# Kernel tuning notes

Measured on AMD Instinct MI355X. Metric: run time of the kernel, lower is better.

The kernel has to match this reference:

```python
import jax, jax.numpy as jnp
import numpy as np

EPSILON = 1e-36


def setup_inputs() -> dict:
    key = jax.random.key(0)
    k1, k2, k3, k4 = jax.random.split(key, 4)
    n, in_dim, out_dim = 8192, 128, 128
    x = jax.random.normal(k1, (n, in_dim), dtype=jnp.float32)
    # xavier-uniform-like scale for W_real
    limit = float(np.sqrt(6.0 / (in_dim + out_dim)))
    W_real = jax.random.uniform(k2, (in_dim, out_dim), dtype=jnp.float32, minval=-limit, maxval=limit)
    W_imag = jax.random.uniform(k3, (in_dim, out_dim), dtype=jnp.float32, minval=-0.1, maxval=0.1)
    G = jax.random.uniform(k4, (in_dim, out_dim), dtype=jnp.float32, minval=0.0, maxval=1.0)
    return {"x": x, "W_real": W_real, "W_imag": W_imag, "G": G}


def reference(x, W_real, W_imag, G):
    Gc = jnp.clip(G, 0.0, 1.0)                                   # (i,o)
    # R: (n,i,o) = |x| gated toward 1 by (1-G)
    R = (jnp.abs(x) + EPSILON)[:, :, None] * Gc[None] + (1.0 - Gc)[None]
    # K: pi where x<0, gated by G
    K = jnp.pi * (x < 0).astype(x.dtype)[:, :, None] * Gc[None]  # (n,i,o)
    logR = jnp.log(R)
    A = jnp.einsum('nio,io->no', logR, W_real) - jnp.einsum('nio,io->no', K, W_imag)
    B = jnp.einsum('nio,io->no', logR, W_imag) + jnp.einsum('nio,io->no', K, W_real)
    return jnp.exp(A) * jnp.cos(B)
```

## Files before the change

kernel.cpp:

```cpp
#include <hip/hip_runtime.h>
#include <math.h>


#define NROWS 8192
#define DIM   128
#define NB    8
#define PI_F  3.14159265358979323846f

typedef float v2f __attribute__((ext_vector_type(2)));

static __device__ __forceinline__ v2f vfma2(v2f a, v2f b, v2f c) {
#if defined(__has_builtin) && __has_builtin(__builtin_elementwise_fma)
    return __builtin_elementwise_fma(a, b, c);
#else
    v2f r; r.x = fmaf(a.x, b.x, c.x); r.y = fmaf(a.y, b.y, c.y); return r;
#endif
}

__global__ __launch_bounds__(256) void prep_kernel(
    const float* __restrict__ x, const float* __restrict__ Wr,
    const float* __restrict__ Wi, const float* __restrict__ G,
    float2* __restrict__ amps, float4* __restrict__ w4)
{
    int idx = blockIdx.x * 256 + threadIdx.x;
    int stride = gridDim.x * 256;
    for (int t = idx; t < NROWS * DIM; t += stride) {
        float xv = x[t];
        float am1 = fabsf(xv) - 1.0f;
        float ps  = (xv < 0.0f) ? PI_F : 0.0f;
        amps[t] = make_float2(am1, ps);
    }
    for (int t = idx; t < DIM * DIM; t += stride) {
        float g = fminf(fmaxf(G[t], 0.0f), 1.0f);
        w4[t] = make_float4(g, Wr[t], Wi[t], 0.0f);
    }
}

__global__ __launch_bounds__(128) void main_kernel(
    const float2* __restrict__ amps, const float4* __restrict__ w4,
    float* __restrict__ out)
{
    const int o = threadIdx.x;
    const int nbase = blockIdx.x * NB;

    v2f accL[NB], accK[NB];
#pragma unroll
    for (int r = 0; r < NB; ++r) { accL[r] = (v2f){0.f, 0.f}; accK[r] = (v2f){0.f, 0.f}; }

    const float2* ap = amps + (size_t)nbase * DIM;

#pragma unroll 2
    for (int i = 0; i < DIM; ++i) {
        float4 w = w4[i * DIM + o];
        const float g = w.x, wr = w.y, wi = w.z;
        const v2f wv = {wr, wi};
        const v2f gv = {g * wi, g * wr};
#pragma unroll
        for (int r = 0; r < NB; ++r) {
            float2 a = ap[r * DIM + i];
            float t  = fmaf(a.x, g, 1.0f);
            float l  = __log2f(t);
            v2f lv = {l, l};
            v2f pv = {a.y, a.y};
            accL[r] = vfma2(lv, wv, accL[r]);
            accK[r] = vfma2(pv, gv, accK[r]);
        }
    }

    const float LN2 = 0.69314718055994530942f;
#pragma unroll
    for (int r = 0; r < NB; ++r) {
        float A = fmaf(LN2, accL[r].x, -accK[r].x);
        float B = fmaf(LN2, accL[r].y,  accK[r].y);
        out[(size_t)(nbase + r) * DIM + o] = expf(A) * cosf(B);
    }
}

__global__ __launch_bounds__(128) void fallback_kernel(
    const float* __restrict__ x, const float* __restrict__ Wr,
    const float* __restrict__ Wi, const float* __restrict__ G,
    float* __restrict__ out)
{
    const int o = threadIdx.x;
    const int nbase = blockIdx.x * NB;

    v2f accL[NB], accK[NB];
#pragma unroll
    for (int r = 0; r < NB; ++r) { accL[r] = (v2f){0.f, 0.f}; accK[r] = (v2f){0.f, 0.f}; }

    for (int i = 0; i < DIM; ++i) {
        float g  = fminf(fmaxf(G[i * DIM + o], 0.0f), 1.0f);
        float wr = Wr[i * DIM + o];
        float wi = Wi[i * DIM + o];
        const v2f wv = {wr, wi};
        const v2f gv = {g * wi, g * wr};
#pragma unroll
        for (int r = 0; r < NB; ++r) {
            float xv  = x[(size_t)(nbase + r) * DIM + i];
            float am1 = fabsf(xv) - 1.0f;
            float ps  = (xv < 0.0f) ? PI_F : 0.0f;
            float t   = fmaf(am1, g, 1.0f);
            float l   = __log2f(t);
            v2f lv = {l, l};
            v2f pv = {ps, ps};
            accL[r] = vfma2(lv, wv, accL[r]);
            accK[r] = vfma2(pv, gv, accK[r]);
        }
    }

    const float LN2 = 0.69314718055994530942f;
#pragma unroll
    for (int r = 0; r < NB; ++r) {
        float A = fmaf(LN2, accL[r].x, -accK[r].x);
        float B = fmaf(LN2, accL[r].y,  accK[r].y);
        out[(size_t)(nbase + r) * DIM + o] = expf(A) * cosf(B);
    }
}

extern "C" void kernel_launch(void* const* d_in, const int* in_sizes, int n_in,
                              void* d_out, int out_size, void* d_ws, size_t ws_size,
                              hipStream_t stream) {
    const float* x  = (const float*)d_in[0];
    const float* Wr = (const float*)d_in[1];
    const float* Wi = (const float*)d_in[2];
    const float* G  = (const float*)d_in[3];
    float* out = (float*)d_out;

    const size_t amps_bytes = (size_t)NROWS * DIM * sizeof(float2);
    const size_t w4_bytes   = (size_t)DIM * DIM * sizeof(float4);
    if (ws_size >= amps_bytes + w4_bytes) {
        float2* amps = (float2*)d_ws;
        float4* w4   = (float4*)((char*)d_ws + amps_bytes);
        prep_kernel<<<1024, 256, 0, stream>>>(x, Wr, Wi, G, amps, w4);
        main_kernel<<<NROWS / NB, 128, 0, stream>>>(amps, w4, out);
    } else {
        fallback_kernel<<<NROWS / NB, 128, 0, stream>>>(x, Wr, Wi, G, out);
    }
}
```

Before: 104.2 us.

## Fuse x preprocessing into main kernel via shared memory, split rows across 512 threads

The per-element x transform (|x|-1 and the sign phase) moves out of a separate global-memory pass and into the main kernel, which stages 8 rows in LDS per block. This drops the write and re-read of an 8 MB intermediate buffer. Each block now has 512 threads, and each thread computes 2 rows for one output column instead of 8. That raises thread-level parallelism but loads each weight float4 four times per block, once per row group.

Measured after the change: 98.12 us. 5.8% less time.

```diff
diff --git a/kernel.cpp b/kernel.cpp
--- a/kernel.cpp
+++ b/kernel.cpp
@@ -4,7 +4,9 @@
 
 #define NROWS 8192
 #define DIM   128
-#define NB    8
+#define RPB   8
+#define NT    512
+#define RPT   2
 #define PI_F  3.14159265358979323846f
 
 typedef float v2f __attribute__((ext_vector_type(2)));
@@ -17,103 +19,76 @@
 #endif
 }
 
-__global__ __launch_bounds__(256) void prep_kernel(
-    const float* __restrict__ x, const float* __restrict__ Wr,
-    const float* __restrict__ Wi, const float* __restrict__ G,
-    float2* __restrict__ amps, float4* __restrict__ w4)
+__global__ __launch_bounds__(256) void prep_w(
+    const float* __restrict__ Wr, const float* __restrict__ Wi,
+    const float* __restrict__ G, float4* __restrict__ w4)
 {
-    int idx = blockIdx.x * 256 + threadIdx.x;
-    int stride = gridDim.x * 256;
-    for (int t = idx; t < NROWS * DIM; t += stride) {
-        float xv = x[t];
-        float am1 = fabsf(xv) - 1.0f;
-        float ps  = (xv < 0.0f) ? PI_F : 0.0f;
-        amps[t] = make_float2(am1, ps);
-    }
-    for (int t = idx; t < DIM * DIM; t += stride) {
+    int t = blockIdx.x * 256 + threadIdx.x;
+    if (t < DIM * DIM) {
         float g = fminf(fmaxf(G[t], 0.0f), 1.0f);
         w4[t] = make_float4(g, Wr[t], Wi[t], 0.0f);
     }
 }
 
-__global__ __launch_bounds__(128) void main_kernel(
-    const float2* __restrict__ amps, const float4* __restrict__ w4,
-    float* __restrict__ out)
+template <bool PACKED>
+__global__ __launch_bounds__(NT, 8) void main_kernel(
+    const float* __restrict__ x, const float4* __restrict__ w4,
+    const float* __restrict__ Wr, const float* __restrict__ Wi,
+    const float* __restrict__ G, float* __restrict__ out)
 {
-    const int o = threadIdx.x;
-    const int nbase = blockIdx.x * NB;
+    __shared__ float2 amps[RPB * DIM];
+    const int tid   = threadIdx.x;
+    const int o     = tid & (DIM - 1);
+    const int q     = tid >> 7;
+    const int nbase = blockIdx.x * RPB;
 
-    v2f accL[NB], accK[NB];
-#pragma unroll
-    for (int r = 0; r < NB; ++r) { accL[r] = (v2f){0.f, 0.f}; accK[r] = (v2f){0.f, 0.f}; }
+    {
+        const float2* xr = (const float2*)(x + (size_t)nbase * DIM);
+        float2 v = xr[tid];
+        float4 s;
+        s.x = fabsf(v.x) - 1.0f;  s.y = (v.x < 0.0f) ? PI_F : 0.0f;
+        s.z = fabsf(v.y) - 1.0f;  s.w = (v.y < 0.0f) ? PI_F : 0.0f;
+        ((float4*)amps)[tid] = s;
+    }
+    __syncthreads();
 
-    const float2* ap = amps + (size_t)nbase * DIM;
+    const float2* ap = amps + q * (RPT * DIM);
+    v2f aL0 = {0.f,0.f}, aK0 = {0.f,0.f}, aL1 = {0.f,0.f}, aK1 = {0.f,0.f};
 
-#pragma unroll 2
+#pragma unroll 4
     for (int i = 0; i < DIM; ++i) {
-        float4 w = w4[i * DIM + o];
-        const float g = w.x, wr = w.y, wi = w.z;
+        float g, wr, wi;
+        if (PACKED) {
+            float4 w = w4[i * DIM + o];
+            g = w.x; wr = w.y; wi = w.z;
+        } else {
+            g  = fminf(fmaxf(G[i * DIM + o], 0.0f), 1.0f);
+            wr = Wr[i * DIM + o]; wi = Wi[i * DIM + o];
+        }
         const v2f wv = {wr, wi};
         const v2f gv = {g * wi, g * wr};
-#pragma unroll
-        for (int r = 0; r < NB; ++r) {
-            float2 a = ap[r * DIM + i];
-            float t  = fmaf(a.x, g, 1.0f);
-            float l  = __log2f(t);
-            v2f lv = {l, l};
-            v2f pv = {a.y, a.y};
-            accL[r] = vfma2(lv, wv, accL[r]);
-            accK[r] = vfma2(pv, gv, accK[r]);
-        }
+        float2 a0 = ap[i];
+        float2 a1 = ap[DIM + i];
+        float t0 = fmaf(a0.x, g, 1.0f);
+        float t1 = fmaf(a1.x, g, 1.0f);
+        float l0 = __log2f(t0);
+        float l1 = __log2f(t1);
+        aL0 = vfma2((v2f){l0, l0},     wv, aL0);
+        aK0 = vfma2((v2f){a0.y, a0.y}, gv, aK0);
+        aL1 = vfma2((v2f){l1, l1},     wv, aL1);
+        aK1 = vfma2((v2f){a1.y, a1.y}, gv, aK1);
     }
 
     const float LN2 = 0.69314718055994530942f;
-#pragma unroll
-    for (int r = 0; r < NB; ++r) {
-        float A = fmaf(LN2, accL[r].x, -accK[r].x);
-        float B = fmaf(LN2, accL[r].y,  accK[r].y);
-        out[(size_t)(nbase + r) * DIM + o] = expf(A) * cosf(B);
+    {
+        float A = fmaf(LN2, aL0.x, -aK0.x);
+        float B = fmaf(LN2, aL0.y,  aK0.y);
+        out[(size_t)(nbase + q * RPT) * DIM + o] = expf(A) * cosf(B);
     }
-}
-
-__global__ __launch_bounds__(128) void fallback_kernel(
-    const float* __restrict__ x, const float* __restrict__ Wr,
-    const float* __restrict__ Wi, const float* __restrict__ G,
-    float* __restrict__ out)
-{
-    const int o = threadIdx.x;
-    const int nbase = blockIdx.x * NB;
-
-    v2f accL[NB], accK[NB];
-#pragma unroll
-    for (int r = 0; r < NB; ++r) { accL[r] = (v2f){0.f, 0.f}; accK[r] = (v2f){0.f, 0.f}; }
-
-    for (int i = 0; i < DIM; ++i) {
-        float g  = fminf(fmaxf(G[i * DIM + o], 0.0f), 1.0f);
-        float wr = Wr[i * DIM + o];
-        float wi = Wi[i * DIM + o];
-        const v2f wv = {wr, wi};
-        const v2f gv = {g * wi, g * wr};
-#pragma unroll
-        for (int r = 0; r < NB; ++r) {
-            float xv  = x[(size_t)(nbase + r) * DIM + i];
-            float am1 = fabsf(xv) - 1.0f;
-            float ps  = (xv < 0.0f) ? PI_F : 0.0f;
-            float t   = fmaf(am1, g, 1.0f);
-            float l   = __log2f(t);
-            v2f lv = {l, l};
-            v2f pv = {ps, ps};
-            accL[r] = vfma2(lv, wv, accL[r]);
-            accK[r] = vfma2(pv, gv, accK[r]);
-        }
-    }
-
-    const float LN2 = 0.69314718055994530942f;
-#pragma unroll
-    for (int r = 0; r < NB; ++r) {
-        float A = fmaf(LN2, accL[r].x, -accK[r].x);
-        float B = fmaf(LN2, accL[r].y,  accK[r].y);
-        out[(size_t)(nbase + r) * DIM + o] = expf(A) * cosf(B);
+    {
+        float A = fmaf(LN2, aL1.x, -aK1.x);
+        float B = fmaf(LN2, aL1.y,  aK1.y);
+        out[(size_t)(nbase + q * RPT + 1) * DIM + o] = expf(A) * cosf(B);
     }
 }
 
@@ -126,14 +101,12 @@
     const float* G  = (const float*)d_in[3];
     float* out = (float*)d_out;
 
-    const size_t amps_bytes = (size_t)NROWS * DIM * sizeof(float2);
-    const size_t w4_bytes   = (size_t)DIM * DIM * sizeof(float4);
-    if (ws_size >= amps_bytes + w4_bytes) {
-        float2* amps = (float2*)d_ws;
-        float4* w4   = (float4*)((char*)d_ws + amps_bytes);
-        prep_kernel<<<1024, 256, 0, stream>>>(x, Wr, Wi, G, amps, w4);
-        main_kernel<<<NROWS / NB, 128, 0, stream>>>(amps, w4, out);
+    const size_t w4_bytes = (size_t)DIM * DIM * sizeof(float4);
+    if (ws_size >= w4_bytes) {
+        float4* w4 = (float4*)d_ws;
+        prep_w<<<(DIM * DIM + 255) / 256, 256, 0, stream>>>(Wr, Wi, G, w4);
+        main_kernel<true><<<NROWS / RPB, NT, 0, stream>>>(x, w4, Wr, Wi, G, out);
     } else {
-        fallback_kernel<<<NROWS / NB, 128, 0, stream>>>(x, Wr, Wi, G, out);
+        main_kernel<false><<<NROWS / RPB, NT, 0, stream>>>(x, nullptr, Wr, Wi, G, out);
     }
 }
```
